# Optimization experiments

Measured on AMD Instinct MI355X. Metric: run time of the kernel, lower is better.

The kernel has to match this reference:

```python
import jax, jax.numpy as jnp
import numpy as np

V = 50000      # word vocab
CV = 128       # char vocab
E = 64         # char embedding size
H = 512        # GRU hidden / word embedding size
T = 20         # max spelling length
B = 2048       # batch of words


def setup_inputs() -> dict:
    key = jax.random.key(0)
    ks = jax.random.split(key, 8)
    chars = jax.random.randint(ks[0], (V, T), 1, CV)
    lengths = jax.random.randint(ks[1], (V,), 1, T + 1)
    mask = jnp.arange(T)[None, :] < lengths[:, None]
    chars = jnp.where(mask, chars, 0)  # padding_idx = 0 beyond each length
    spelling_table = jnp.concatenate([chars, lengths[:, None]], axis=1).astype(jnp.int32)
    data = jax.random.randint(ks[2], (B,), 0, V).astype(jnp.int32)
    s = 1.0 / np.sqrt(H)
    emb = (jax.random.normal(ks[3], (CV, E), jnp.float32) * 0.1).at[0].set(0.0)
    W_ih = jax.random.uniform(ks[4], (3 * H, E), jnp.float32, -s, s)
    W_hh = jax.random.uniform(ks[5], (3 * H, H), jnp.float32, -s, s)
    b_ih = jax.random.uniform(ks[6], (3 * H,), jnp.float32, -s, s)
    b_hh = jax.random.uniform(ks[7], (3 * H,), jnp.float32, -s, s)
    return {"data": data, "spelling_table": spelling_table, "emb": emb,
            "W_ih": W_ih, "W_hh": W_hh, "b_ih": b_ih, "b_hh": b_hh}


def reference(data, spelling_table, emb, W_ih, W_hh, b_ih, b_hh):
    H_ = W_hh.shape[1]
    rec = spelling_table[data]            # [B, T+1] gather of spellings
    spelling = rec[:, :-1]                # [B, T] char ids
    lengths = rec[:, -1]                  # [B]
    # torch.sort(lengths, descending=True): stable descending argsort
    perm = jnp.argsort(-lengths)
    sorted_sp = spelling[perm]            # [B, T]
    sorted_len = lengths[perm]            # [B]
    x = emb[sorted_sp]                    # [B, T, E]
    # precompute input projections for all timesteps (fused r|z|n gates)
    xW = jnp.einsum('bte,ge->btg', x, W_ih) + b_ih   # [B, T, 3H]
    valid = (jnp.arange(x.shape[1])[None, :] < sorted_len[:, None])  # [B, T]

    def step(h, inp):
        xw_t, v_t = inp                   # [B, 3H], [B, 1]
        hW = h @ W_hh.T + b_hh            # [B, 3H]
        xr, xz, xn = jnp.split(xw_t, 3, axis=-1)
        hr, hz, hn = jnp.split(hW, 3, axis=-1)
        r = jax.nn.sigmoid(xr + hr)
        z = jax.nn.sigmoid(xz + hz)
        n = jnp.tanh(xn + r * hn)
        h_new = (1.0 - z) * n + z * h
        h = jnp.where(v_t, h_new, h)      # packed-sequence semantics
        return h, None

    h0 = jnp.zeros((x.shape[0], H_), x.dtype)
    ht, _ = jax.lax.scan(step, h0, (jnp.swapaxes(xW, 0, 1), valid.T[:, :, None]))
    # faithful reproduction of the original's unsort: ht[sorted_length_idx]
    return ht[perm]
```

## Files before the change

### kernel.cpp

```cpp
#include <hip/hip_runtime.h>
#include <hip/hip_bf16.h>
#include <math.h>

#define B_  2048
#define E_  64
#define H_  512
#define T_  20

typedef _Float16 half8 __attribute__((ext_vector_type(8)));
typedef __attribute__((ext_vector_type(4))) float f32x4;
typedef unsigned long long u64;

#define mf16(a, b, c) __builtin_amdgcn_mfma_f32_16x16x32_f16(a, b, c, 0, 0, 0)

__device__ __forceinline__ float sigmoidf_(float x) {
  return 1.0f / (1.0f + __expf(-x));
}
__device__ __forceinline__ float tanh_fast(float x) {
  float e = __expf(2.0f * x);
  return 1.0f - 2.0f / (e + 1.0f);
}

__global__ __launch_bounds__(256) void k_setup(const int* __restrict__ data,
                                               const int* __restrict__ st,
                                               int* __restrict__ perm,
                                               int* __restrict__ iperm,
                                               int* __restrict__ Mt,
                                               int* __restrict__ flags) {
  __shared__ int lens[B_];
  __shared__ int hist[256][22];
  __shared__ int sub[16][22];
  __shared__ int subpre[16][22];
  __shared__ int cnt[32];
  __shared__ int offs[32];
  int tid = threadIdx.x;

  #pragma unroll
  for (int i = 0; i < 4; ++i) flags[tid * 4 + i] = 0;

  #pragma unroll
  for (int q = 0; q < 8; ++q) {
    int i = tid * 8 + q;
    lens[i] = st[data[i] * (T_ + 1) + T_];
  }
  #pragma unroll
  for (int L = 0; L < 22; ++L) hist[tid][L] = 0;
  #pragma unroll
  for (int q = 0; q < 8; ++q) hist[tid][lens[tid * 8 + q]]++;
  __syncthreads();

  for (int q = tid; q < 16 * 21; q += 256) {
    int g = q / 21, L = q % 21;
    int run = 0;
    for (int j = 0; j < 16; ++j) {
      int v = hist[g * 16 + j][L];
      hist[g * 16 + j][L] = run;
      run += v;
    }
    sub[g][L] = run;
  }
  __syncthreads();
  if (tid < 21) {
    int run = 0;
    for (int g = 0; g < 16; ++g) { subpre[g][tid] = run; run += sub[g][tid]; }
    cnt[tid] = run;
  }
  __syncthreads();
  if (tid <= 20) {
    int s = 0;
    for (int L = tid + 1; L <= 20; ++L) s += cnt[L];
    offs[tid] = s;
  }
  __syncthreads();
  if (tid < T_) Mt[tid] = offs[tid];
  if (tid >= T_ && tid < 32) Mt[tid] = 0;

  int g = tid >> 4;
  #pragma unroll
  for (int q = 0; q < 8; ++q) {
    int i = tid * 8 + q;
    int L = lens[i];
    int rk = subpre[g][L] + hist[tid][L];
    hist[tid][L] += 1;
    perm[offs[L] + rk] = i;
  }
  __syncthreads();
  #pragma unroll
  for (int q = 0; q < 8; ++q) {
    int i = tid * 8 + q;
    iperm[perm[i]] = i;
  }
}

__global__ void k_schars(const int* __restrict__ data, const int* __restrict__ st,
                         const int* __restrict__ perm, int* __restrict__ schars_T) {
  int idx = blockIdx.x * 256 + threadIdx.x;
  if (idx >= B_ * T_) return;
  int t = idx >> 11;
  int j = idx & (B_ - 1);
  schars_T[idx] = st[data[perm[j]] * (T_ + 1) + t];
}

__global__ void k_wconv(const float* __restrict__ W_hh, _Float16* __restrict__ Wp) {
  int idx = blockIdx.x * 256 + threadIdx.x;
  if (idx >= 8 * 16 * 12 * 512) return;
  int e = idx & 7;
  int l = (idx >> 3) & 63;
  int rest = idx >> 9;
  int g = rest % 3;  rest /= 3;
  int wc = rest & 3; rest >>= 2;
  int c = rest % 16;
  int cb = rest / 16;
  int grow = g * H_ + cb * 64 + wc * 16 + (l & 15);
  int k = c * 32 + (l >> 4) * 8 + e;
  Wp[idx] = (_Float16)W_hh[grow * H_ + k];
}

__global__ __launch_bounds__(256) void k_embw(const float* __restrict__ emb,
                                              const float* __restrict__ W_ih,
                                              const float* __restrict__ b_ih,
                                              const float* __restrict__ b_hh,
                                              float* __restrict__ embW) {
  int c = blockIdx.x;
  int tid = threadIdx.x;
  __shared__ float ev[64];
  if (tid < 64) ev[tid] = emb[c * E_ + tid];
  __syncthreads();
  for (int o = tid; o < 3 * H_; o += 256) {
    float s = b_ih[o];
    if (o < 2 * H_) s += b_hh[o];
    #pragma unroll
    for (int k = 0; k < E_; ++k) s = fmaf(ev[k], W_ih[o * E_ + k], s);
    embW[(size_t)c * (3 * H_) + o] = s;
  }
}

__global__ __launch_bounds__(256, 1) void k_gru(
    const int* __restrict__ Mt, const int* __restrict__ schars_T,
    const float* __restrict__ embW, const _Float16* __restrict__ Wp,
    const float* __restrict__ b_hh,
    _Float16* __restrict__ hq0, _Float16* __restrict__ hq1,
    const int* __restrict__ iperm, float* __restrict__ out,
    int* __restrict__ bar) {
  __shared__ __attribute__((aligned(16))) _Float16 As[64][512];
  __shared__ __attribute__((aligned(16))) _Float16 Hs[64][68];

  int bid = blockIdx.x;
  int rb = bid & 31, cb = bid >> 5;
  int m0 = rb * 64;
  int tid = threadIdx.x;
  int w = tid >> 6;
  int l = tid & 63;
  int ln = l & 15, kc = l >> 4;

  int colg = cb * 64 + w * 16 + ln;
  float bnh = b_hh[2 * H_ + colg];

  float hreg[4][4];
  #pragma unroll
  for (int i = 0; i < 4; ++i)
    #pragma unroll
    for (int j = 0; j < 4; ++j) hreg[i][j] = 0.0f;

  int* barp = bar + rb * 32;

#define WLOAD(c, g) (*(const half8*)(Wp + \
    (((size_t)(cb * 16 + (c)) * 4 + w) * 3 + (g)) * 512 + l * 8))

#define H_CHUNK(c, F, FB)                                                      \
  {                                                                            \
    _Pragma("unroll")                                                          \
    for (int rf = 0; rf < 4; ++rf) {                                           \
      int r = rf * 16 + ln;                                                    \
      half8 af = *(const half8*)((const _Float16*)As + r * 512 +               \
                                 ((((c) * 4 + kc) ^ (ln & 7)) << 3));          \
      accr[rf]  = mf16(af, F[((c) - (FB)) * 3 + 0], accr[rf]);                 \
      accz[rf]  = mf16(af, F[((c) - (FB)) * 3 + 1], accz[rf]);                 \
      accnh[rf] = mf16(af, F[((c) - (FB)) * 3 + 2], accnh[rf]);                \
    }                                                                          \
  }

  for (int t = 0; t < T_; ++t) {
    int M = Mt[t];
    if (m0 >= M) break;
    const _Float16* hin = (t & 1) ? hq1 : hq0;
    _Float16*       hout = (t & 1) ? hq0 : hq1;

    int chv[4][4];
    #pragma unroll
    for (int rf = 0; rf < 4; ++rf)
      #pragma unroll
      for (int q = 0; q < 4; ++q)
        chv[rf][q] = schars_T[t * B_ + m0 + rf * 16 + kc * 4 + q];

    f32x4 accr[4], accz[4], accnh[4];
    #pragma unroll
    for (int i = 0; i < 4; ++i) {
      accr[i] = (f32x4){0.f, 0.f, 0.f, 0.f};
      accz[i] = (f32x4){0.f, 0.f, 0.f, 0.f};
      accnh[i] = (f32x4){0.f, 0.f, 0.f, 0.f};
    }

    if (t > 0) {
      if (tid == 0) {
        int target = 8 * t;
        while (__hip_atomic_load(barp, __ATOMIC_RELAXED, __HIP_MEMORY_SCOPE_AGENT) < target) {}
      }
      __syncthreads();
      u64 sb[16][2];
      #pragma unroll
      for (int i = 0; i < 16; ++i) {
        int r = w * 16 + i;
        u64* src = (u64*)(hin + (size_t)(m0 + r) * H_) + ((l ^ (i & 7)) << 1);
        sb[i][0] = __hip_atomic_load(src, __ATOMIC_RELAXED, __HIP_MEMORY_SCOPE_AGENT);
        sb[i][1] = __hip_atomic_load(src + 1, __ATOMIC_RELAXED, __HIP_MEMORY_SCOPE_AGENT);
      }

      half8 wfA[12], wfB[12];
      #pragma unroll
      for (int cc = 0; cc < 4; ++cc)
        #pragma unroll
        for (int g = 0; g < 3; ++g) {
          wfA[cc * 3 + g] = WLOAD(cc, g);
          wfB[cc * 3 + g] = WLOAD(4 + cc, g);
        }

      #pragma unroll
      for (int i = 0; i < 16; ++i) {
        int r = w * 16 + i;
        u64* dp = (u64*)&As[r][l * 8];
        dp[0] = sb[i][0];
        dp[1] = sb[i][1];
      }
      __syncthreads();

      H_CHUNK(0, wfA, 0) H_CHUNK(1, wfA, 0) H_CHUNK(2, wfA, 0) H_CHUNK(3, wfA, 0)
      __builtin_amdgcn_sched_barrier(0);
      #pragma unroll
      for (int cc = 0; cc < 4; ++cc)
        #pragma unroll
        for (int g = 0; g < 3; ++g)
          wfA[cc * 3 + g] = WLOAD(8 + cc, g);
      H_CHUNK(4, wfB, 4) H_CHUNK(5, wfB, 4) H_CHUNK(6, wfB, 4) H_CHUNK(7, wfB, 4)
      __builtin_amdgcn_sched_barrier(0);
      #pragma unroll
      for (int cc = 0; cc < 4; ++cc)
        #pragma unroll
        for (int g = 0; g < 3; ++g)
          wfB[cc * 3 + g] = WLOAD(12 + cc, g);
      H_CHUNK(8, wfA, 8) H_CHUNK(9, wfA, 8) H_CHUNK(10, wfA, 8) H_CHUNK(11, wfA, 8)
      __builtin_amdgcn_sched_barrier(0);
      H_CHUNK(12, wfB, 12) H_CHUNK(13, wfB, 12) H_CHUNK(14, wfB, 12) H_CHUNK(15, wfB, 12)
    } else {
      __syncthreads();
    }

    #pragma unroll
    for (int rf = 0; rf < 4; ++rf) {
      #pragma unroll
      for (int q = 0; q < 4; ++q) {
        int row_l = rf * 16 + kc * 4 + q;
        if (m0 + row_l < M) {
          const float* ew = embW + (size_t)chv[rf][q] * (3 * H_) + colg;
          float r_ = sigmoidf_(accr[rf][q] + ew[0]);
          float z_ = sigmoidf_(accz[rf][q] + ew[H_]);
          float n_ = tanh_fast(ew[2 * H_] + r_ * (accnh[rf][q] + bnh));
          float hnew = (1.0f - z_) * n_ + z_ * hreg[rf][q];
          hreg[rf][q] = hnew;
          Hs[row_l][w * 16 + ln] = (_Float16)hnew;
        }
      }
    }
    __syncthreads();

    #pragma unroll
    for (int j = 0; j < 4; ++j) {
      int c = tid + 256 * j;
      int row_l = c >> 4;
      int coff = (c & 15) * 4;
      if (m0 + row_l < M) {
        u64 v = *(const u64*)&Hs[row_l][coff];
        __hip_atomic_store((u64*)(hout + (size_t)(m0 + row_l) * H_ + cb * 64 + coff),
                           v, __ATOMIC_RELAXED, __HIP_MEMORY_SCOPE_AGENT);
      }
    }
    asm volatile("s_waitcnt vmcnt(0)" ::: "memory");
    __syncthreads();
    if (tid == 0)
      __hip_atomic_fetch_add(barp, 1, __ATOMIC_RELAXED, __HIP_MEMORY_SCOPE_AGENT);
  }
#undef H_CHUNK
#undef WLOAD

  #pragma unroll
  for (int rf = 0; rf < 4; ++rf) {
    #pragma unroll
    for (int q = 0; q < 4; ++q) {
      int row = m0 + rf * 16 + kc * 4 + q;
      out[(size_t)iperm[row] * H_ + colg] = hreg[rf][q];
    }
  }
}

extern "C" void kernel_launch(void* const* d_in, const int* in_sizes, int n_in,
                              void* d_out, int out_size, void* d_ws, size_t ws_size,
                              hipStream_t stream) {
  const int*   data = (const int*)d_in[0];
  const int*   st   = (const int*)d_in[1];
  const float* emb  = (const float*)d_in[2];
  const float* W_ih = (const float*)d_in[3];
  const float* W_hh = (const float*)d_in[4];
  const float* b_ih = (const float*)d_in[5];
  const float* b_hh = (const float*)d_in[6];
  float* out = (float*)d_out;

  _Float16* hq0  = (_Float16*)d_ws;
  _Float16* hq1  = hq0 + B_ * H_;
  _Float16* Wp   = hq1 + B_ * H_;
  float*    embW = (float*)(Wp + 8 * 16 * 12 * 512);
  int* perm   = (int*)(embW + 128 * 3 * H_);
  int* iperm  = perm + B_;
  int* Mt     = iperm + B_;
  int* flags  = Mt + 32;
  int* schars = flags + 1024;

  k_setup<<<1, 256, 0, stream>>>(data, st, perm, iperm, Mt, flags);
  k_schars<<<(B_ * T_ + 255) / 256, 256, 0, stream>>>(data, st, perm, schars);
  k_wconv<<<(8 * 16 * 12 * 512 + 255) / 256, 256, 0, stream>>>(W_hh, Wp);
  k_embw<<<128, 256, 0, stream>>>(emb, W_ih, b_ih, b_hh, embW);

  k_gru<<<dim3(256), dim3(256), 0, stream>>>(Mt, schars, embW, Wp, b_hh,
                                             hq0, hq1, iperm, out, flags);
}
```

Measured before the change: 229.9 us.

## Split GRU K-dimension across two wave groups with register-resident W_hh

The recurrent kernel now launches 512 threads per block. Each half of the waves handles half of the hidden K dimension and keeps its W_hh fragments resident in registers for all timesteps, instead of reloading them from global memory every step. Partial sums are exchanged through a new shared-memory reduction buffer, and the gate epilogue is split so each wave group finishes half the rows. This removes per-step weight reloads and doubles the wave count, at the cost of an extra LDS round trip, an extra barrier per step, and higher register pressure.

```diff
diff --git a/kernel.cpp b/kernel.cpp
--- a/kernel.cpp
+++ b/kernel.cpp
@@ -135,7 +135,7 @@
   }
 }
 
-__global__ __launch_bounds__(256, 1) void k_gru(
+__global__ __launch_bounds__(512, 1) void k_gru(
     const int* __restrict__ Mt, const int* __restrict__ schars_T,
     const float* __restrict__ embW, const _Float16* __restrict__ Wp,
     const float* __restrict__ b_hh,
@@ -143,55 +143,67 @@
     const int* __restrict__ iperm, float* __restrict__ out,
     int* __restrict__ bar) {
   __shared__ __attribute__((aligned(16))) _Float16 As[64][512];
+  __shared__ __attribute__((aligned(16))) float    Rs[3][64][68];
   __shared__ __attribute__((aligned(16))) _Float16 Hs[64][68];
 
   int bid = blockIdx.x;
   int rb = bid & 31, cb = bid >> 5;
   int m0 = rb * 64;
   int tid = threadIdx.x;
-  int w = tid >> 6;
-  int l = tid & 63;
-  int ln = l & 15, kc = l >> 4;
-
-  int colg = cb * 64 + w * 16 + ln;
+  int w  = tid >> 6;
+  int wc = w & 3, kh = w >> 2;
+  int l  = tid & 63, ln = l & 15, kc = l >> 4;
+
+  half8 wfr[24];
+  #pragma unroll
+  for (int f = 0; f < 8; ++f)
+    #pragma unroll
+    for (int g = 0; g < 3; ++g)
+      wfr[f * 3 + g] = *(const half8*)(Wp +
+          (((size_t)(cb * 16 + kh * 8 + f) * 4 + wc) * 3 + g) * 512 + l * 8);
+
+  int colg = cb * 64 + wc * 16 + ln;
+  int colw = wc * 16 + ln;
   float bnh = b_hh[2 * H_ + colg];
 
-  float hreg[4][4];
-  #pragma unroll
-  for (int i = 0; i < 4; ++i)
+  float hreg[2][4];
+  #pragma unroll
+  for (int i = 0; i < 2; ++i)
     #pragma unroll
     for (int j = 0; j < 4; ++j) hreg[i][j] = 0.0f;
 
   int* barp = bar + rb * 32;
 
-#define WLOAD(c, g) (*(const half8*)(Wp + \
-    (((size_t)(cb * 16 + (c)) * 4 + w) * 3 + (g)) * 512 + l * 8))
-
-#define H_CHUNK(c, F, FB)                                                      \
+#define EPI(RF, D, ROWB)                                                       \
   {                                                                            \
+    f32x4 pr4, pz4, pn4;                                                       \
+    if (t > 0) {                                                               \
+      pr4 = *(const f32x4*)&Rs[0][colw][(ROWB)];                               \
+      pz4 = *(const f32x4*)&Rs[1][colw][(ROWB)];                               \
+      pn4 = *(const f32x4*)&Rs[2][colw][(ROWB)];                               \
+    } else {                                                                   \
+      pr4 = (f32x4){0.f, 0.f, 0.f, 0.f}; pz4 = pr4; pn4 = pr4;                 \
+    }                                                                          \
     _Pragma("unroll")                                                          \
-    for (int rf = 0; rf < 4; ++rf) {                                           \
-      int r = rf * 16 + ln;                                                    \
-      half8 af = *(const half8*)((const _Float16*)As + r * 512 +               \
-                                 ((((c) * 4 + kc) ^ (ln & 7)) << 3));          \
-      accr[rf]  = mf16(af, F[((c) - (FB)) * 3 + 0], accr[rf]);                 \
-      accz[rf]  = mf16(af, F[((c) - (FB)) * 3 + 1], accz[rf]);                 \
-      accnh[rf] = mf16(af, F[((c) - (FB)) * 3 + 2], accnh[rf]);                \
+    for (int q = 0; q < 4; ++q) {                                              \
+      int row_l = (ROWB) + q;                                                  \
+      if (m0 + row_l < M) {                                                    \
+        int chv = schars_T[t * B_ + m0 + row_l];                               \
+        const float* ew = embW + (size_t)chv * (3 * H_) + colg;                \
+        float r_ = sigmoidf_(accr[RF][q] + pr4[q] + ew[0]);                    \
+        float z_ = sigmoidf_(accz[RF][q] + pz4[q] + ew[H_]);                   \
+        float n_ = tanh_fast(ew[2 * H_] + r_ * (accnh[RF][q] + pn4[q] + bnh)); \
+        hreg[D][q] = (1.0f - z_) * n_ + z_ * hreg[D][q];                       \
+        Hs[row_l][colw] = (_Float16)hreg[D][q];                                \
+      }                                                                        \
     }                                                                          \
   }
 
   for (int t = 0; t < T_; ++t) {
     int M = Mt[t];
     if (m0 >= M) break;
-    const _Float16* hin = (t & 1) ? hq1 : hq0;
+    const _Float16* hin  = (t & 1) ? hq1 : hq0;
     _Float16*       hout = (t & 1) ? hq0 : hq1;
-
-    int chv[4][4];
-    #pragma unroll
-    for (int rf = 0; rf < 4; ++rf)
-      #pragma unroll
-      for (int q = 0; q < 4; ++q)
-        chv[rf][q] = schars_T[t * B_ + m0 + rf * 16 + kc * 4 + q];
 
     f32x4 accr[4], accz[4], accnh[4];
     #pragma unroll
@@ -207,75 +219,67 @@
         while (__hip_atomic_load(barp, __ATOMIC_RELAXED, __HIP_MEMORY_SCOPE_AGENT) < target) {}
       }
       __syncthreads();
-      u64 sb[16][2];
+      u64 sb[8][2];
       #pragma unroll
-      for (int i = 0; i < 16; ++i) {
-        int r = w * 16 + i;
+      for (int i = 0; i < 8; ++i) {
+        int r = w * 8 + i;
         u64* src = (u64*)(hin + (size_t)(m0 + r) * H_) + ((l ^ (i & 7)) << 1);
         sb[i][0] = __hip_atomic_load(src, __ATOMIC_RELAXED, __HIP_MEMORY_SCOPE_AGENT);
         sb[i][1] = __hip_atomic_load(src + 1, __ATOMIC_RELAXED, __HIP_MEMORY_SCOPE_AGENT);
       }
-
-      half8 wfA[12], wfB[12];
       #pragma unroll
-      for (int cc = 0; cc < 4; ++cc)
-        #pragma unroll
-        for (int g = 0; g < 3; ++g) {
-          wfA[cc * 3 + g] = WLOAD(cc, g);
-          wfB[cc * 3 + g] = WLOAD(4 + cc, g);
-        }
-
-      #pragma unroll
-      for (int i = 0; i < 16; ++i) {
-        int r = w * 16 + i;
+      for (int i = 0; i < 8; ++i) {
+        int r = w * 8 + i;
         u64* dp = (u64*)&As[r][l * 8];
         dp[0] = sb[i][0];
         dp[1] = sb[i][1];
       }
       __syncthreads();
 
-      H_CHUNK(0, wfA, 0) H_CHUNK(1, wfA, 0) H_CHUNK(2, wfA, 0) H_CHUNK(3, wfA, 0)
-      __builtin_amdgcn_sched_barrier(0);
       #pragma unroll
-      for (int cc = 0; cc < 4; ++cc)
+      for (int f = 0; f < 8; ++f) {
+        int chk = kh * 8 + f;
         #pragma unroll
-        for (int g = 0; g < 3; ++g)
-          wfA[cc * 3 + g] = WLOAD(8 + cc, g);
-      H_CHUNK(4, wfB, 4) H_CHUNK(5, wfB, 4) H_CHUNK(6, wfB, 4) H_CHUNK(7, wfB, 4)
-      __builtin_amdgcn_sched_barrier(0);
-      #pragma unroll
-      for (int cc = 0; cc < 4; ++cc)
-        #pragma unroll
-        for (int g = 0; g < 3; ++g)
-          wfB[cc * 3 + g] = WLOAD(12 + cc, g);
-      H_CHUNK(8, wfA, 8) H_CHUNK(9, wfA, 8) H_CHUNK(10, wfA, 8) H_CHUNK(11, wfA, 8)
-      __builtin_amdgcn_sched_barrier(0);
-      H_CHUNK(12, wfB, 12) H_CHUNK(13, wfB, 12) H_CHUNK(14, wfB, 12) H_CHUNK(15, wfB, 12)
+        for (int rf = 0; rf < 4; ++rf) {
+          int r = rf * 16 + ln;
+          half8 af = *(const half8*)((const _Float16*)As + r * 512 +
+                                     (((chk * 4 + kc) ^ (ln & 7)) << 3));
+          accr[rf]  = mf16(af, wfr[f * 3 + 0], accr[rf]);
+          accz[rf]  = mf16(af, wfr[f * 3 + 1], accz[rf]);
+          accnh[rf] = mf16(af, wfr[f * 3 + 2], accnh[rf]);
+        }
+      }
+
+      if (kh == 0) {
+        *(f32x4*)&Rs[0][colw][32 + kc * 4] = accr[2];
+        *(f32x4*)&Rs[1][colw][32 + kc * 4] = accz[2];
+        *(f32x4*)&Rs[2][colw][32 + kc * 4] = accnh[2];
+        *(f32x4*)&Rs[0][colw][48 + kc * 4] = accr[3];
+        *(f32x4*)&Rs[1][colw][48 + kc * 4] = accz[3];
+        *(f32x4*)&Rs[2][colw][48 + kc * 4] = accnh[3];
+      } else {
+        *(f32x4*)&Rs[0][colw][0 + kc * 4]  = accr[0];
+        *(f32x4*)&Rs[1][colw][0 + kc * 4]  = accz[0];
+        *(f32x4*)&Rs[2][colw][0 + kc * 4]  = accnh[0];
+        *(f32x4*)&Rs[0][colw][16 + kc * 4] = accr[1];
+        *(f32x4*)&Rs[1][colw][16 + kc * 4] = accz[1];
+        *(f32x4*)&Rs[2][colw][16 + kc * 4] = accnh[1];
+      }
+      __syncthreads();
+    }
+
+    if (kh == 0) {
+      EPI(0, 0, kc * 4)
+      EPI(1, 1, 16 + kc * 4)
     } else {
-      __syncthreads();
-    }
-
-    #pragma unroll
-    for (int rf = 0; rf < 4; ++rf) {
-      #pragma unroll
-      for (int q = 0; q < 4; ++q) {
-        int row_l = rf * 16 + kc * 4 + q;
-        if (m0 + row_l < M) {
-          const float* ew = embW + (size_t)chv[rf][q] * (3 * H_) + colg;
-          float r_ = sigmoidf_(accr[rf][q] + ew[0]);
-          float z_ = sigmoidf_(accz[rf][q] + ew[H_]);
-          float n_ = tanh_fast(ew[2 * H_] + r_ * (accnh[rf][q] + bnh));
-          float hnew = (1.0f - z_) * n_ + z_ * hreg[rf][q];
-          hreg[rf][q] = hnew;
-          Hs[row_l][w * 16 + ln] = (_Float16)hnew;
-        }
-      }
+      EPI(2, 0, 32 + kc * 4)
+      EPI(3, 1, 48 + kc * 4)
     }
     __syncthreads();
 
     #pragma unroll
-    for (int j = 0; j < 4; ++j) {
-      int c = tid + 256 * j;
+    for (int j = 0; j < 2; ++j) {
+      int c = tid + 512 * j;
       int row_l = c >> 4;
       int coff = (c & 15) * 4;
       if (m0 + row_l < M) {
@@ -289,15 +293,14 @@
     if (tid == 0)
       __hip_atomic_fetch_add(barp, 1, __ATOMIC_RELAXED, __HIP_MEMORY_SCOPE_AGENT);
   }
-#undef H_CHUNK
-#undef WLOAD
-
-  #pragma unroll
-  for (int rf = 0; rf < 4; ++rf) {
+#undef EPI
+
+  #pragma unroll
+  for (int d = 0; d < 2; ++d) {
     #pragma unroll
     for (int q = 0; q < 4; ++q) {
-      int row = m0 + rf * 16 + kc * 4 + q;
-      out[(size_t)iperm[row] * H_ + colg] = hreg[rf][q];
+      int row = m0 + (kh * 32 + d * 16) + kc * 4 + q;
+      out[(size_t)iperm[row] * H_ + colg] = hreg[d][q];
     }
   }
 }
@@ -329,6 +332,6 @@
   k_wconv<<<(8 * 16 * 12 * 512 + 255) / 256, 256, 0, stream>>>(W_hh, Wp);
   k_embw<<<128, 256, 0, stream>>>(emb, W_ih, b_ih, b_hh, embW);
 
-  k_gru<<<dim3(256), dim3(256), 0, stream>>>(Mt, schars, embW, Wp, b_hh,
+  k_gru<<<dim3(256), dim3(512), 0, stream>>>(Mt, schars, embW, Wp, b_hh,
                                              hq0, hq1, iperm, out, flags);
 }
```

Result: faster. 188.5 us (-18.0%).
